# Performance work log

Measured on AMD Instinct MI355X. Metric: run time of the kernel, lower is better.

Reference implementation:

```python
import jax, jax.numpy as jnp
import numpy as np

N_FEAT = 7          # input_vector_size
M = 3               # memberships per feature (hardcoded 3 in torch module)
FUZZ = M ** N_FEAT  # 2187, cartesian product size
MID = 512
NUM_CLASS = 10
BATCH = 4096

# Precompute cartesian-product index table: itertools.product over rows of u[i]
# (last feature index varies fastest). IDX[k, i] = which of the 3 memberships of
# feature i appears in combination k.
_k = np.arange(FUZZ)
IDX = ((_k[:, None] // (M ** np.arange(N_FEAT - 1, -1, -1))[None, :]) % M).astype(np.int32)  # [FUZZ, N_FEAT]


def setup_inputs() -> dict:
    key = jax.random.key(0)
    ks = jax.random.split(key, 8)
    x = jax.random.normal(ks[0], (BATCH, N_FEAT), dtype=jnp.float32)
    # Parameters (xavier-ish init for weights, ones for b/bais as in torch init)
    c = jax.random.uniform(ks[1], (N_FEAT, M), minval=-1.0, maxval=1.0, dtype=jnp.float32)
    b = jnp.ones((N_FEAT, M), dtype=jnp.float32)
    wei = jax.random.uniform(ks[2], (FUZZ * N_FEAT, FUZZ), minval=-0.01, maxval=0.01, dtype=jnp.float32)
    bais = jnp.ones((1,), dtype=jnp.float32)
    W1 = jax.random.normal(ks[3], (MID, FUZZ), dtype=jnp.float32) * (1.0 / np.sqrt(FUZZ))
    b1 = jnp.zeros((MID,), dtype=jnp.float32)
    W2 = jax.random.normal(ks[4], (FUZZ, MID), dtype=jnp.float32) * (1.0 / np.sqrt(MID))
    b2 = jnp.zeros((FUZZ,), dtype=jnp.float32)
    W3 = jax.random.normal(ks[5], (NUM_CLASS, FUZZ), dtype=jnp.float32) * (1.0 / np.sqrt(FUZZ))
    b3 = jnp.zeros((NUM_CLASS,), dtype=jnp.float32)
    return {"x": x, "c": c, "b": b, "wei": wei, "bais": bais,
            "W1": W1, "b1": b1, "W2": W2, "b2": b2, "W3": W3, "b3": b3}


def reference(x, c, b, wei, bais, W1, b1, W2, b2, W3, b3):
    B = x.shape[0]
    # Gaussian fuzzy memberships: u[b, i, j] = exp(-(x[b,i]-c[i,j])^2 / b[i,j]^2)
    u = jnp.exp(-((x[:, :, None] - c[None]) ** 2) / (b[None] ** 2))  # [B, N_FEAT, M]
    # Cartesian product: dd[bt, k, i] = u[bt, i, IDX[k, i]]  (replaces itertools.product)
    idx = jnp.asarray(IDX)                       # [FUZZ, N_FEAT]
    feat = jnp.arange(N_FEAT)[None, :]           # [1, N_FEAT] broadcasts to [FUZZ, N_FEAT]
    dd = u[:, feat, idx]                         # [B, FUZZ, N_FEAT]
    # Fuzzy rule layer
    a = dd.reshape(B, FUZZ * N_FEAT) @ wei + bais            # [B, FUZZ]
    a_mean = a / jnp.sum(a, axis=1, keepdims=True)
    # Small residual MLP
    h1 = a_mean @ W1.T + b1                                   # [B, MID]
    h2 = h1 @ W2.T + b2                                       # [B, FUZZ]
    h3 = (a_mean + h2) @ W3.T + b3                            # [B, NUM_CLASS]
    out = jax.nn.leaky_relu(h3, negative_slope=0.2)
    # Dropout(0.5) omitted (eval mode / deterministic baseline)
    return out
```

## Files before the change

kernel.cpp:

```cpp
#include <hip/hip_runtime.h>

#define FUZZ 2187
#define NFEAT 7
#define MID 512
#define NCLS 10
#define BATCH 4096
#define SSTR 2192

__global__ __launch_bounds__(256) void k_reduce_wei(const float* __restrict__ wei,
                                                    float* __restrict__ S) {
    int n = blockIdx.x * 256 + threadIdx.x;
    if (n >= FUZZ) return;
    float acc[21];
#pragma unroll
    for (int t = 0; t < 21; ++t) acc[t] = 0.f;
    int k0 = blockIdx.y * 27;
    for (int kk = 0; kk < 27; ++kk) {
        int k = k0 + kk;
        int t = k;
        int d[7];
        d[6] = t % 3; t /= 3;
        d[5] = t % 3; t /= 3;
        d[4] = t % 3; t /= 3;
        d[3] = t % 3; t /= 3;
        d[2] = t % 3; t /= 3;
        d[1] = t % 3; t /= 3;
        d[0] = t;
        const float* rowp = wei + (size_t)(k * 7) * FUZZ + n;
#pragma unroll
        for (int j = 0; j < 7; ++j) {
            float v = rowp[(size_t)j * FUZZ];
            int m = d[j];
            acc[j * 3 + 0] += (m == 0) ? v : 0.f;
            acc[j * 3 + 1] += (m == 1) ? v : 0.f;
            acc[j * 3 + 2] += (m == 2) ? v : 0.f;
        }
    }
#pragma unroll
    for (int t = 0; t < 21; ++t)
        atomicAdd(&S[t * SSTR + n], acc[t]);
}

__device__ __forceinline__ float wave_sum(float v) {
#pragma unroll
    for (int off = 32; off > 0; off >>= 1) v += __shfl_down(v, off, 64);
    return v;
}

__global__ __launch_bounds__(64) void k_sw1(const float* __restrict__ S,
                                            const float* __restrict__ W1,
                                            float* __restrict__ SW1,
                                            float* __restrict__ ws1) {
    int i = blockIdx.x;
    int lane = threadIdx.x;
    float acc[21];
    float aw = 0.f;
#pragma unroll
    for (int t = 0; t < 21; ++t) acc[t] = 0.f;
    for (int n = lane; n < FUZZ; n += 64) {
        float w1 = W1[(size_t)i * FUZZ + n];
        aw += w1;
#pragma unroll
        for (int t = 0; t < 21; ++t) acc[t] += S[t * SSTR + n] * w1;
    }
#pragma unroll
    for (int t = 0; t < 21; ++t) acc[t] = wave_sum(acc[t]);
    aw = wave_sum(aw);
    if (lane == 0) {
#pragma unroll
        for (int t = 0; t < 21; ++t) SW1[t * MID + i] = acc[t];
        ws1[i] = aw;
    }
}

__global__ __launch_bounds__(64) void k_g(const float* __restrict__ SW1,
                                          const float* __restrict__ ws1,
                                          const float* __restrict__ b1,
                                          const float* __restrict__ W2,
                                          float* __restrict__ G,
                                          float* __restrict__ q,
                                          float* __restrict__ p) {
    int n = blockIdx.x;
    int lane = threadIdx.x;
    float acc[21];
    float aq = 0.f, ap = 0.f;
#pragma unroll
    for (int t = 0; t < 21; ++t) acc[t] = 0.f;
    for (int i = lane; i < MID; i += 64) {
        float w2 = W2[(size_t)n * MID + i];
        aq += ws1[i] * w2;
        ap += b1[i] * w2;
#pragma unroll
        for (int t = 0; t < 21; ++t) acc[t] += SW1[t * MID + i] * w2;
    }
#pragma unroll
    for (int t = 0; t < 21; ++t) acc[t] = wave_sum(acc[t]);
    aq = wave_sum(aq);
    ap = wave_sum(ap);
    if (lane == 0) {
#pragma unroll
        for (int t = 0; t < 21; ++t) G[t * SSTR + n] = acc[t];
        q[n] = aq;
        p[n] = ap;
    }
}

__global__ __launch_bounds__(64) void k_h(const float* __restrict__ S,
                                          const float* __restrict__ G,
                                          const float* __restrict__ q,
                                          const float* __restrict__ p,
                                          const float* __restrict__ b2,
                                          const float* __restrict__ b3,
                                          const float* __restrict__ W3,
                                          float* __restrict__ H,
                                          float* __restrict__ v,
                                          float* __restrict__ w,
                                          float* __restrict__ T) {
    int c = blockIdx.x;
    int lane = threadIdx.x;
    if (c < NCLS) {
        float acc[21];
        float av = 0.f, aw = 0.f;
#pragma unroll
        for (int t = 0; t < 21; ++t) acc[t] = 0.f;
        for (int n = lane; n < FUZZ; n += 64) {
            float w3 = W3[(size_t)c * FUZZ + n];
            av += (1.0f + q[n]) * w3;
            aw += (p[n] + b2[n]) * w3;
#pragma unroll
            for (int t = 0; t < 21; ++t)
                acc[t] += (S[t * SSTR + n] + G[t * SSTR + n]) * w3;
        }
#pragma unroll
        for (int t = 0; t < 21; ++t) acc[t] = wave_sum(acc[t]);
        av = wave_sum(av);
        aw = wave_sum(aw);
        if (lane == 0) {
#pragma unroll
            for (int t = 0; t < 21; ++t) H[t * NCLS + c] = acc[t];
            v[c] = av;
            w[c] = aw + b3[c];
        }
    } else {
        float acc[21];
#pragma unroll
        for (int t = 0; t < 21; ++t) acc[t] = 0.f;
        for (int n = lane; n < FUZZ; n += 64) {
#pragma unroll
            for (int t = 0; t < 21; ++t) acc[t] += S[t * SSTR + n];
        }
#pragma unroll
        for (int t = 0; t < 21; ++t) acc[t] = wave_sum(acc[t]);
        if (lane == 0) {
#pragma unroll
            for (int t = 0; t < 21; ++t) T[t] = acc[t];
        }
    }
}

__global__ __launch_bounds__(256) void k_out(const float* __restrict__ x,
                                             const float* __restrict__ cc,
                                             const float* __restrict__ bbv,
                                             const float* __restrict__ bais,
                                             const float* __restrict__ T,
                                             const float* __restrict__ H,
                                             const float* __restrict__ v,
                                             const float* __restrict__ w,
                                             float* __restrict__ out) {
    int b = blockIdx.x * 256 + threadIdx.x;
    if (b >= BATCH) return;
    float xv[NFEAT];
#pragma unroll
    for (int j = 0; j < NFEAT; ++j) xv[j] = x[b * NFEAT + j];
    float u[21];
#pragma unroll
    for (int j = 0; j < NFEAT; ++j) {
#pragma unroll
        for (int m = 0; m < 3; ++m) {
            float d = xv[j] - cc[j * 3 + m];
            float bv = bbv[j * 3 + m];
            u[j * 3 + m] = expf(-(d * d) / (bv * bv));
        }
    }
    float ba = bais[0];
    float r = 2187.0f * ba;
#pragma unroll
    for (int t = 0; t < 21; ++t) r += u[t] * T[t];
    float inv = 1.0f / r;
#pragma unroll
    for (int c = 0; c < NCLS; ++c) {
        float s = 0.f;
#pragma unroll
        for (int t = 0; t < 21; ++t) s += u[t] * H[t * NCLS + c];
        float h = (s + ba * v[c]) * inv + w[c];
        out[b * NCLS + c] = (h >= 0.f) ? h : 0.2f * h;
    }
}

extern "C" void kernel_launch(void* const* d_in, const int* in_sizes, int n_in,
                              void* d_out, int out_size, void* d_ws, size_t ws_size,
                              hipStream_t stream) {
    const float* x    = (const float*)d_in[0];
    const float* c    = (const float*)d_in[1];
    const float* bbv  = (const float*)d_in[2];
    const float* wei  = (const float*)d_in[3];
    const float* bais = (const float*)d_in[4];
    const float* W1   = (const float*)d_in[5];
    const float* b1   = (const float*)d_in[6];
    const float* W2   = (const float*)d_in[7];
    const float* b2   = (const float*)d_in[8];
    const float* W3   = (const float*)d_in[9];
    const float* b3   = (const float*)d_in[10];

    float* ws  = (float*)d_ws;
    float* S   = ws;
    float* G   = S + 21 * SSTR;
    float* SW1 = G + 21 * SSTR;
    float* ws1 = SW1 + 21 * MID;
    float* q   = ws1 + MID;
    float* p   = q + SSTR;
    float* T   = p + SSTR;
    float* H   = T + 32;
    float* v   = H + 224;
    float* w   = v + 16;

    hipMemsetAsync(S, 0, (size_t)(21 * SSTR) * sizeof(float), stream);
    k_reduce_wei<<<dim3(9, 81), 256, 0, stream>>>(wei, S);
    k_sw1<<<MID, 64, 0, stream>>>(S, W1, SW1, ws1);
    k_g<<<FUZZ, 64, 0, stream>>>(SW1, ws1, b1, W2, G, q, p);
    k_h<<<NCLS + 1, 64, 0, stream>>>(S, G, q, p, b2, b3, W3, H, v, w, T);
    k_out<<<(BATCH + 255) / 256, 256, 0, stream>>>(x, c, bbv, bais, T, H, v, w,
                                                   (float*)d_out);
}
```

Measured before the change: 303.4 us.

## Replace atomic wei reduction with partial-sum buffer and second reduce pass

The first-stage reduction over the large wei matrix stops using 21 atomicAdds per thread into a zeroed buffer. It now writes 13 per-chunk partial rows, exploiting the fact that within a 27-row chunk the first four digits are constant, and a new k_reduce2 kernel sums the partials into S. This removes the memset and the atomics. k_sw1 and k_h also move from one wave to 256 and 512 threads per block with shared-memory cross-wave reduction, to raise parallelism in those small-grid kernels. The change adds an extra launch and a partial buffer of about 9 MB.

```diff
diff --git a/kernel.cpp b/kernel.cpp
--- a/kernel.cpp
+++ b/kernel.cpp
@@ -6,39 +6,86 @@
 #define NCLS 10
 #define BATCH 4096
 #define SSTR 2192
+#define NCHUNK 81
+#define PROWS 13
 
 __global__ __launch_bounds__(256) void k_reduce_wei(const float* __restrict__ wei,
-                                                    float* __restrict__ S) {
+                                                    float* __restrict__ Spart) {
     int n = blockIdx.x * 256 + threadIdx.x;
     if (n >= FUZZ) return;
-    float acc[21];
-#pragma unroll
-    for (int t = 0; t < 21; ++t) acc[t] = 0.f;
-    int k0 = blockIdx.y * 27;
+    int by = blockIdx.y;
+
+    float sum4[4];
+    float acc9[9];
+#pragma unroll
+    for (int j = 0; j < 4; ++j) sum4[j] = 0.f;
+#pragma unroll
+    for (int r = 0; r < 9; ++r) acc9[r] = 0.f;
+
+    const float* base = wei + (size_t)(by * 27) * 7 * FUZZ + n;
+#pragma unroll
     for (int kk = 0; kk < 27; ++kk) {
-        int k = k0 + kk;
-        int t = k;
-        int d[7];
-        d[6] = t % 3; t /= 3;
-        d[5] = t % 3; t /= 3;
-        d[4] = t % 3; t /= 3;
-        d[3] = t % 3; t /= 3;
-        d[2] = t % 3; t /= 3;
-        d[1] = t % 3; t /= 3;
-        d[0] = t;
-        const float* rowp = wei + (size_t)(k * 7) * FUZZ + n;
-#pragma unroll
-        for (int j = 0; j < 7; ++j) {
-            float v = rowp[(size_t)j * FUZZ];
-            int m = d[j];
-            acc[j * 3 + 0] += (m == 0) ? v : 0.f;
-            acc[j * 3 + 1] += (m == 1) ? v : 0.f;
-            acc[j * 3 + 2] += (m == 2) ? v : 0.f;
-        }
-    }
-#pragma unroll
-    for (int t = 0; t < 21; ++t)
-        atomicAdd(&S[t * SSTR + n], acc[t]);
+        const float* rp = base + (size_t)kk * 7 * FUZZ;
+        float v0 = rp[0];
+        float v1 = rp[(size_t)1 * FUZZ];
+        float v2 = rp[(size_t)2 * FUZZ];
+        float v3 = rp[(size_t)3 * FUZZ];
+        float v4 = rp[(size_t)4 * FUZZ];
+        float v5 = rp[(size_t)5 * FUZZ];
+        float v6 = rp[(size_t)6 * FUZZ];
+        sum4[0] += v0;
+        sum4[1] += v1;
+        sum4[2] += v2;
+        sum4[3] += v3;
+        acc9[0 + (kk / 9)]       += v4;
+        acc9[3 + ((kk / 3) % 3)] += v5;
+        acc9[6 + (kk % 3)]       += v6;
+    }
+
+    float* outp = Spart + (size_t)by * PROWS * FUZZ + n;
+#pragma unroll
+    for (int j = 0; j < 4; ++j) outp[(size_t)j * FUZZ] = sum4[j];
+#pragma unroll
+    for (int r = 0; r < 9; ++r) outp[(size_t)(4 + r) * FUZZ] = acc9[r];
+}
+
+__global__ __launch_bounds__(256) void k_reduce2(const float* __restrict__ Spart,
+                                                 float* __restrict__ S) {
+    int n = blockIdx.x * 256 + threadIdx.x;
+    if (n >= FUZZ) return;
+    int t = blockIdx.y;
+    float s;
+    if (t < 12) {
+        int j = t / 3, m = t % 3;
+        const int places[4] = {27, 9, 3, 1};
+        int ops[3];
+        int o = 0;
+#pragma unroll
+        for (int q = 0; q < 4; ++q)
+            if (q != j) ops[o++] = places[q];
+        int byb = m * places[j];
+        float s0 = 0.f, s1 = 0.f, s2 = 0.f;
+#pragma unroll 9
+        for (int c = 0; c < 27; c += 3) {
+            int by0 = byb + (c / 9) * ops[0] + (((c + 0) / 3) % 3) * ops[1] + ((c + 0) % 3) * ops[2];
+            int by1 = byb + (c / 9) * ops[0] + (((c + 1) / 3) % 3) * ops[1] + ((c + 1) % 3) * ops[2];
+            int by2 = byb + (c / 9) * ops[0] + (((c + 2) / 3) % 3) * ops[1] + ((c + 2) % 3) * ops[2];
+            s0 += Spart[((size_t)by0 * PROWS + j) * FUZZ + n];
+            s1 += Spart[((size_t)by1 * PROWS + j) * FUZZ + n];
+            s2 += Spart[((size_t)by2 * PROWS + j) * FUZZ + n];
+        }
+        s = s0 + s1 + s2;
+    } else {
+        int row = t - 8;
+        float s0 = 0.f, s1 = 0.f, s2 = 0.f;
+        for (int by = 0; by < 81; by += 3) {
+            s0 += Spart[((size_t)(by + 0) * PROWS + row) * FUZZ + n];
+            s1 += Spart[((size_t)(by + 1) * PROWS + row) * FUZZ + n];
+            s2 += Spart[((size_t)(by + 2) * PROWS + row) * FUZZ + n];
+        }
+        s = s0 + s1 + s2;
+    }
+    S[t * SSTR + n] = s;
 }
 
 __device__ __forceinline__ float wave_sum(float v) {
@@ -47,17 +94,17 @@
     return v;
 }
 
-__global__ __launch_bounds__(64) void k_sw1(const float* __restrict__ S,
-                                            const float* __restrict__ W1,
-                                            float* __restrict__ SW1,
-                                            float* __restrict__ ws1) {
+__global__ __launch_bounds__(256) void k_sw1(const float* __restrict__ S,
+                                             const float* __restrict__ W1,
+                                             float* __restrict__ SW1,
+                                             float* __restrict__ ws1) {
     int i = blockIdx.x;
-    int lane = threadIdx.x;
+    int tid = threadIdx.x;
     float acc[21];
     float aw = 0.f;
 #pragma unroll
     for (int t = 0; t < 21; ++t) acc[t] = 0.f;
-    for (int n = lane; n < FUZZ; n += 64) {
+    for (int n = tid; n < FUZZ; n += 256) {
         float w1 = W1[(size_t)i * FUZZ + n];
         aw += w1;
 #pragma unroll
@@ -66,10 +113,18 @@
 #pragma unroll
     for (int t = 0; t < 21; ++t) acc[t] = wave_sum(acc[t]);
     aw = wave_sum(aw);
+    __shared__ float red[4][22];
+    int w = tid >> 6, lane = tid & 63;
     if (lane == 0) {
 #pragma unroll
-        for (int t = 0; t < 21; ++t) SW1[t * MID + i] = acc[t];
-        ws1[i] = aw;
+        for (int t = 0; t < 21; ++t) red[w][t] = acc[t];
+        red[w][21] = aw;
+    }
+    __syncthreads();
+    if (tid < 22) {
+        float v = red[0][tid] + red[1][tid] + red[2][tid] + red[3][tid];
+        if (tid < 21) SW1[tid * MID + i] = v;
+        else          ws1[i] = v;
     }
 }
 
@@ -105,25 +160,27 @@
     }
 }
 
-__global__ __launch_bounds__(64) void k_h(const float* __restrict__ S,
-                                          const float* __restrict__ G,
-                                          const float* __restrict__ q,
-                                          const float* __restrict__ p,
-                                          const float* __restrict__ b2,
-                                          const float* __restrict__ b3,
-                                          const float* __restrict__ W3,
-                                          float* __restrict__ H,
-                                          float* __restrict__ v,
-                                          float* __restrict__ w,
-                                          float* __restrict__ T) {
+__global__ __launch_bounds__(512) void k_h(const float* __restrict__ S,
+                                           const float* __restrict__ G,
+                                           const float* __restrict__ q,
+                                           const float* __restrict__ p,
+                                           const float* __restrict__ b2,
+                                           const float* __restrict__ b3,
+                                           const float* __restrict__ W3,
+                                           float* __restrict__ H,
+                                           float* __restrict__ v,
+                                           float* __restrict__ w,
+                                           float* __restrict__ T) {
     int c = blockIdx.x;
-    int lane = threadIdx.x;
+    int tid = threadIdx.x;
+    int wv = tid >> 6, lane = tid & 63;
+    __shared__ float red[8][24];
+    float acc[21];
+#pragma unroll
+    for (int t = 0; t < 21; ++t) acc[t] = 0.f;
     if (c < NCLS) {
-        float acc[21];
         float av = 0.f, aw = 0.f;
-#pragma unroll
-        for (int t = 0; t < 21; ++t) acc[t] = 0.f;
-        for (int n = lane; n < FUZZ; n += 64) {
+        for (int n = tid; n < FUZZ; n += 512) {
             float w3 = W3[(size_t)c * FUZZ + n];
             av += (1.0f + q[n]) * w3;
             aw += (p[n] + b2[n]) * w3;
@@ -137,15 +194,21 @@
         aw = wave_sum(aw);
         if (lane == 0) {
 #pragma unroll
-            for (int t = 0; t < 21; ++t) H[t * NCLS + c] = acc[t];
-            v[c] = av;
-            w[c] = aw + b3[c];
+            for (int t = 0; t < 21; ++t) red[wv][t] = acc[t];
+            red[wv][21] = av;
+            red[wv][22] = aw;
+        }
+        __syncthreads();
+        if (tid < 23) {
+            float s = 0.f;
+#pragma unroll
+            for (int k = 0; k < 8; ++k) s += red[k][tid];
+            if (tid < 21)      H[tid * NCLS + c] = s;
+            else if (tid == 21) v[c] = s;
+            else               w[c] = s + b3[c];
         }
     } else {
-        float acc[21];
-#pragma unroll
-        for (int t = 0; t < 21; ++t) acc[t] = 0.f;
-        for (int n = lane; n < FUZZ; n += 64) {
+        for (int n = tid; n < FUZZ; n += 512) {
 #pragma unroll
             for (int t = 0; t < 21; ++t) acc[t] += S[t * SSTR + n];
         }
@@ -153,7 +216,14 @@
         for (int t = 0; t < 21; ++t) acc[t] = wave_sum(acc[t]);
         if (lane == 0) {
 #pragma unroll
-            for (int t = 0; t < 21; ++t) T[t] = acc[t];
+            for (int t = 0; t < 21; ++t) red[wv][t] = acc[t];
+        }
+        __syncthreads();
+        if (tid < 21) {
+            float s = 0.f;
+#pragma unroll
+            for (int k = 0; k < 8; ++k) s += red[k][tid];
+            T[tid] = s;
         }
     }
 }
@@ -212,23 +282,24 @@
     const float* W3   = (const float*)d_in[9];
     const float* b3   = (const float*)d_in[10];
 
-    float* ws  = (float*)d_ws;
-    float* S   = ws;
-    float* G   = S + 21 * SSTR;
-    float* SW1 = G + 21 * SSTR;
-    float* ws1 = SW1 + 21 * MID;
-    float* q   = ws1 + MID;
-    float* p   = q + SSTR;
-    float* T   = p + SSTR;
-    float* H   = T + 32;
-    float* v   = H + 224;
-    float* w   = v + 16;
-
-    hipMemsetAsync(S, 0, (size_t)(21 * SSTR) * sizeof(float), stream);
-    k_reduce_wei<<<dim3(9, 81), 256, 0, stream>>>(wei, S);
-    k_sw1<<<MID, 64, 0, stream>>>(S, W1, SW1, ws1);
+    float* ws    = (float*)d_ws;
+    float* Spart = ws;
+    float* S     = Spart + 2302912;
+    float* G     = S + 21 * SSTR;
+    float* SW1   = G + 21 * SSTR;
+    float* ws1   = SW1 + 21 * MID;
+    float* q     = ws1 + MID;
+    float* p     = q + SSTR;
+    float* T     = p + SSTR;
+    float* H     = T + 32;
+    float* v     = H + 224;
+    float* w     = v + 16;
+
+    k_reduce_wei<<<dim3(9, NCHUNK), 256, 0, stream>>>(wei, Spart);
+    k_reduce2<<<dim3(9, 21), 256, 0, stream>>>(Spart, S);
+    k_sw1<<<MID, 256, 0, stream>>>(S, W1, SW1, ws1);
     k_g<<<FUZZ, 64, 0, stream>>>(SW1, ws1, b1, W2, G, q, p);
-    k_h<<<NCLS + 1, 64, 0, stream>>>(S, G, q, p, b2, b3, W3, H, v, w, T);
+    k_h<<<NCLS + 1, 512, 0, stream>>>(S, G, q, p, b2, b3, W3, H, v, w, T);
     k_out<<<(BATCH + 255) / 256, 256, 0, stream>>>(x, c, bbv, bais, T, H, v, w,
                                                    (float*)d_out);
 }
```

Result: slower. 310.0 us (+2.2%).
